# Kernel tuning notes

Hardware: AMD Instinct MI355X
Metric: run time of the kernel (lower is better)

## Reference

```python
import jax, jax.numpy as jnp
import numpy as np

N_NODES = 100000
N_HEDGES = 10000
D = 128  # i_d = v_d = e_d = q_d
NUM_CLASS = 10
E = 640000


def _linear_params(key, d_in, d_out):
    k1, k2 = jax.random.split(key)
    lim = 1.0 / np.sqrt(d_in)
    W = jax.random.uniform(k1, (d_in, d_out), jnp.float32, -lim, lim)
    b = jax.random.uniform(k2, (d_out,), jnp.float32, -lim, lim)
    return W, b


def setup_inputs() -> dict:
    key = jax.random.key(0)
    ks = jax.random.split(key, 12)
    vfeat = jax.random.normal(ks[0], (N_NODES, D), jnp.float32)
    efeat = jax.random.normal(ks[1], (N_HEDGES, D), jnp.float32)
    he_idx = jax.random.randint(ks[2], (E,), 0, N_HEDGES, jnp.int32)
    nd_idx = jax.random.randint(ks[3], (E,), 0, N_NODES, jnp.int32)
    Wfl, bfl = _linear_params(ks[4], D, D)   # first_layer_in: i_d -> v_d
    W1, b1 = _linear_params(ks[5], D, D)     # w1: e_d -> q_d
    W2, b2 = _linear_params(ks[6], D, D)     # w2: v_d -> q_d
    W3, b3 = _linear_params(ks[7], D, D)     # w3: v_d -> e_d
    W4, b4 = _linear_params(ks[8], D, D)     # w4: v_d -> q_d
    W5, b5 = _linear_params(ks[9], D, D)     # w5: e_d -> q_d
    W6, b6 = _linear_params(ks[10], D, D)    # w6: e_d -> v_d
    Wc, bc = _linear_params(ks[11], D, NUM_CLASS)
    return dict(vfeat=vfeat, efeat=efeat, he_idx=he_idx, nd_idx=nd_idx,
                first_layer=1, last_layer=1,
                Wfl=Wfl, bfl=bfl, W1=W1, b1=b1, W2=W2, b2=b2, W3=W3, b3=b3,
                W4=W4, b4=b4, W5=W5, b5=b5, W6=W6, b6=b6, Wc=Wc, bc=bc)


def _segment_softmax(logits, segs, num_segments):
    # softmax over the variable-size mailbox of each destination segment
    m = jax.ops.segment_max(logits, segs, num_segments=num_segments)
    m = jnp.where(jnp.isfinite(m), m, 0.0)  # empty segments
    e = jnp.exp(logits - m[segs])
    s = jax.ops.segment_sum(e, segs, num_segments=num_segments)
    return e / jnp.where(s > 0, s, 1.0)[segs]


def reference(vfeat, efeat, he_idx, nd_idx, first_layer, last_layer,
              Wfl, bfl, W1, b1, W2, b2, W3, b3, W4, b4, W5, b5, W6, b6, Wc, bc):
    scale = 1.0 / np.sqrt(D).astype(np.float32)
    # first_layer path (first_layer=1)
    feat_e = efeat @ Wfl + bfl                         # [M, v_d]
    k_e = feat_e @ W5 + b5                             # [M, q_d]
    v_e = feat_e @ W6 + b6                             # [M, v_d]
    q_v = vfeat @ W4 + b4                              # [N, q_d]
    # etype 'con': hyperedge -> node
    attn1 = jax.nn.leaky_relu((k_e[he_idx] * q_v[nd_idx]).sum(-1)) * scale  # [E]
    a1 = _segment_softmax(attn1, nd_idx, N_NODES)
    feat_v = jax.ops.segment_sum(a1[:, None] * v_e[he_idx], nd_idx,
                                 num_segments=N_NODES)  # [N, v_d]
    # etype 'in': node -> hyperedge
    k_v = feat_v @ W2 + b2                             # [N, q_d]
    v_v = feat_v @ W3 + b3                             # [N, e_d]
    q_e = feat_e @ W1 + b1                             # [M, q_d]
    attn2 = jax.nn.leaky_relu((k_v[nd_idx] * q_e[he_idx]).sum(-1)) * scale  # [E]
    a2 = _segment_softmax(attn2, he_idx, N_HEDGES)
    feat_e2 = jax.ops.segment_sum(a2[:, None] * v_v[nd_idx], he_idx,
                                  num_segments=N_HEDGES)  # [M, e_d]
    # last_layer path (last_layer=1): classification head (file save omitted)
    pred = feat_e2 @ Wc + bc                           # [M, num_class]
    return pred
```

## Files before the change

kernel.cpp:

```cpp
#include <hip/hip_runtime.h>
#include <hip/hip_bf16.h>
#include <math.h>


#define HY_M 10000
#define HY_N 100000
#define HY_E 640000

#define SH_N 9
#define NB_N 196
#define SH_M 6
#define NB_M 157

typedef float        f32x4 __attribute__((ext_vector_type(4)));
typedef unsigned int u32x4 __attribute__((ext_vector_type(4)));

__device__ __forceinline__ unsigned int f2bf(float x) {
    unsigned int u = __float_as_uint(x);
    return (u + 0x7fffu + ((u >> 16) & 1u)) >> 16;
}
__device__ __forceinline__ float2 bf2x2(unsigned int w) {
    float lo = __uint_as_float(w << 16);
    float hi = __uint_as_float(w & 0xffff0000u);
    return make_float2(lo, hi);
}
__device__ __forceinline__ float dot8(uint4 kw, float4 qa, float4 qb) {
    float2 k0 = bf2x2(kw.x), k1 = bf2x2(kw.y), k2 = bf2x2(kw.z), k3 = bf2x2(kw.w);
    return k0.x * qa.x + k0.y * qa.y + k1.x * qa.z + k1.y * qa.w
         + k2.x * qb.x + k2.y * qb.y + k3.x * qb.z + k3.y * qb.w;
}
__device__ __forceinline__ void unpack8(uint4 vw, float (&vf)[8]) {
    float2 v0 = bf2x2(vw.x), v1 = bf2x2(vw.y), v2 = bf2x2(vw.z), v3 = bf2x2(vw.w);
    vf[0] = v0.x; vf[1] = v0.y; vf[2] = v1.x; vf[3] = v1.y;
    vf[4] = v2.x; vf[5] = v2.y; vf[6] = v3.x; vf[7] = v3.y;
}
__device__ __forceinline__ float red16(float d) {
    d += __shfl_xor(d, 8); d += __shfl_xor(d, 4);
    d += __shfl_xor(d, 2); d += __shfl_xor(d, 1);
    return d;
}

__launch_bounds__(256)
__global__ void coarse_hist(const int* __restrict__ nd, const int* __restrict__ he,
                            int* __restrict__ gcntN, int* __restrict__ gcntM, int E) {
    __shared__ int hN[256], hM[256];
    const int t = threadIdx.x;
    hN[t] = 0; hM[t] = 0;
    __syncthreads();
    const int base = blockIdx.x * 1024;
    for (int i = t; i < 1024; i += 256) {
        int e = base + i;
        if (e < E) {
            atomicAdd(&hN[nd[e] >> SH_N], 1);
            atomicAdd(&hM[he[e] >> SH_M], 1);
        }
    }
    __syncthreads();
    if (hN[t]) atomicAdd(&gcntN[t], hN[t]);
    if (hM[t]) atomicAdd(&gcntM[t], hM[t]);
}

__global__ void coarse_scan(const int* __restrict__ gcntN, const int* __restrict__ gcntM,
                            int* __restrict__ coffN, int* __restrict__ coffM, int E) {
    __shared__ int s[256];
    const int* g = blockIdx.x ? gcntM : gcntN;
    int* o = blockIdx.x ? coffM : coffN;
    const int nb = blockIdx.x ? NB_M : NB_N;
    const int t = threadIdx.x;
    int v = (t < nb) ? g[t] : 0;
    int orig = v;
    s[t] = v; __syncthreads();
    for (int off = 1; off < 256; off <<= 1) {
        int x = (t >= off) ? s[t - off] : 0;
        __syncthreads(); s[t] += x; __syncthreads();
    }
    if (t < nb) o[t] = s[t] - orig;
    if (t == 0) o[nb] = E;
}

__launch_bounds__(256)
__global__ void part_scatter(const int* __restrict__ nd, const int* __restrict__ he,
                             const int* __restrict__ coffN, const int* __restrict__ coffM,
                             int* __restrict__ gcurN, int* __restrict__ gcurM,
                             unsigned int* __restrict__ stN, unsigned int* __restrict__ stM,
                             int E) {
    __shared__ int hN[256], hM[256];
    const int t = threadIdx.x;
    hN[t] = 0; hM[t] = 0;
    __syncthreads();
    const int base = blockIdx.x * 1024;
    for (int i = t; i < 1024; i += 256) {
        int e = base + i;
        if (e < E) {
            atomicAdd(&hN[nd[e] >> SH_N], 1);
            atomicAdd(&hM[he[e] >> SH_M], 1);
        }
    }
    __syncthreads();
    int cN = hN[t], cM = hM[t];
    __syncthreads();
    if (cN) hN[t] = coffN[t] + atomicAdd(&gcurN[t], cN);
    if (cM) hM[t] = coffM[t] + atomicAdd(&gcurM[t], cM);
    __syncthreads();
    for (int i = t; i < 1024; i += 256) {
        int e = base + i;
        if (e < E) {
            int d = nd[e], h = he[e];
            int pN = atomicAdd(&hN[d >> SH_N], 1);
            stN[pN] = ((unsigned int)(d & 511) << 14) | (unsigned int)h;
            int pM = atomicAdd(&hM[h >> SH_M], 1);
            stM[pM] = ((unsigned int)(h & 63) << 17) | (unsigned int)d;
        }
    }
}

__launch_bounds__(256)
__global__ void bucket_build(const unsigned int* __restrict__ stN,
                             const unsigned int* __restrict__ stM,
                             const int* __restrict__ coffN, const int* __restrict__ coffM,
                             int* __restrict__ nd_off, int* __restrict__ he_off,
                             int* __restrict__ nd_adj, int* __restrict__ he_adj,
                             int* __restrict__ dcntg) {
    __shared__ int cnt[512];
    __shared__ int cur[512];
    __shared__ int ps[256];
    __shared__ int dh[64];
    int b = blockIdx.x;
    const int t = threadIdx.x;
    const unsigned int* st; const int* coff; int* offout; int* adj;
    int dmin, dcnt2, sshift; unsigned int smask; int ntot;
    const bool isN = b < NB_N;
    if (isN) {
        st = stN; coff = coffN; offout = nd_off; adj = nd_adj;
        dmin = b << SH_N; dcnt2 = min(512, HY_N - dmin);
        sshift = 14; smask = 0x3FFFu; ntot = HY_N;
    } else {
        b -= NB_N;
        st = stM; coff = coffM; offout = he_off; adj = he_adj;
        dmin = b << SH_M; dcnt2 = min(64, HY_M - dmin);
        sshift = 17; smask = 0x1FFFFu; ntot = HY_M;
    }
    const int cbase = coff[b], cend = coff[b + 1];
    cnt[t] = 0; cnt[t + 256] = 0;
    if (t < 64) dh[t] = 0;
    __syncthreads();
    for (int k = cbase + t; k < cend; k += 256)
        atomicAdd(&cnt[st[k] >> sshift], 1);
    __syncthreads();
    int a0 = cnt[2 * t], a1 = cnt[2 * t + 1];
    int pair = a0 + a1;
    ps[t] = pair;
    __syncthreads();
    for (int off = 1; off < 256; off <<= 1) {
        int x = (t >= off) ? ps[t - off] : 0;
        __syncthreads(); ps[t] += x; __syncthreads();
    }
    int excl = ps[t] - pair;
    cur[2 * t]     = cbase + excl;
    cur[2 * t + 1] = cbase + excl + a0;
    __syncthreads();
    for (int i = t; i < dcnt2; i += 256) offout[dmin + i] = cur[i];
    if (t == 0 && dmin + dcnt2 == ntot) offout[ntot] = cend;
    if (isN) {
        for (int i = t; i < dcnt2; i += 256)
            atomicAdd(&dh[min(cnt[i], 63)], 1);
    }
    __syncthreads();
    if (isN && t < 64 && dh[t]) atomicAdd(&dcntg[t], dh[t]);
    for (int k = cbase + t; k < cend; k += 256) {
        unsigned int w = st[k];
        int pos = atomicAdd(&cur[w >> sshift], 1);
        adj[pos] = (int)(w & smask);
    }
}

__global__ void deg_scan(const int* __restrict__ dcnt, int* __restrict__ dcur) {
    int t = threadIdx.x;
    int rt = 63 - t;
    int v = dcnt[rt];
    int s = v;
    for (int o = 1; o < 64; o <<= 1) {
        int x = __shfl_up(s, o, 64);
        if (t >= o) s += x;
    }
    dcur[rt] = s - v;
}

__launch_bounds__(256)
__global__ void deg_scatter(const int* __restrict__ off, int* __restrict__ dcur,
                            int* __restrict__ nperm, int n) {
    __shared__ int h[64];
    __shared__ int basev[64];
    int t = threadIdx.x;
    if (t < 64) h[t] = 0;
    __syncthreads();
    int i = blockIdx.x * blockDim.x + t;
    int bin = 0, lpos = 0;
    bool valid = i < n;
    if (valid) {
        bin = min(off[i + 1] - off[i], 63);
        lpos = atomicAdd(&h[bin], 1);
    }
    __syncthreads();
    if (t < 64 && h[t]) basev[t] = atomicAdd(&dcur[t], h[t]);
    __syncthreads();
    if (valid) nperm[basev[bin] + lpos] = i;
}

__device__ __forceinline__ void gemm_accum(const float* __restrict__ A,
        const float* __restrict__ W, int nrows, float* wlds,
        float (&acc)[4][4], int row0) {
    const int tid = threadIdx.x;
    const int cg = tid & 31;
    for (int i = tid; i < 4096; i += 512)
        ((float4*)wlds)[i] = ((const float4*)W)[i];
    __syncthreads();
    const float4* A0 = (const float4*)(A + (size_t)min(row0 + 0, nrows - 1) * 128);
    const float4* A1 = (const float4*)(A + (size_t)min(row0 + 1, nrows - 1) * 128);
    const float4* A2 = (const float4*)(A + (size_t)min(row0 + 2, nrows - 1) * 128);
    const float4* A3 = (const float4*)(A + (size_t)min(row0 + 3, nrows - 1) * 128);
    #pragma unroll 2
    for (int kq = 0; kq < 32; ++kq) {
        float4 ar[4] = {A0[kq], A1[kq], A2[kq], A3[kq]};
        const float4* wk = (const float4*)(wlds + kq * 512);
        float4 wr[4] = {wk[cg], wk[32 + cg], wk[64 + cg], wk[96 + cg]};
        #pragma unroll
        for (int r = 0; r < 4; ++r) {
            float av[4] = {ar[r].x, ar[r].y, ar[r].z, ar[r].w};
            #pragma unroll
            for (int j = 0; j < 4; ++j) {
                float wv[4] = {wr[j].x, wr[j].y, wr[j].z, wr[j].w};
                #pragma unroll
                for (int c = 0; c < 4; ++c)
                    acc[r][c] = fmaf(av[j], wv[c], acc[r][c]);
            }
        }
    }
}

__device__ __forceinline__ void gemm_store_f32(const float* __restrict__ b,
        float* __restrict__ Cf, int nrows, float (&acc)[4][4], int row0) {
    const int cg = threadIdx.x & 31;
    const float4 bv = ((const float4*)b)[cg];
    #pragma unroll
    for (int r = 0; r < 4; ++r) {
        int gr = row0 + r;
        if (gr < nrows) {
            float4 o = {acc[r][0] + bv.x, acc[r][1] + bv.y,
                        acc[r][2] + bv.z, acc[r][3] + bv.w};
            ((float4*)(Cf + (size_t)gr * 128))[cg] = o;
        }
    }
}

__launch_bounds__(512)
__global__ void gemm_pair(const float* __restrict__ Aa, const float* __restrict__ Wa,
                          float* __restrict__ Ca,
                          const float* __restrict__ Ab, const float* __restrict__ Wb,
                          float* __restrict__ Cb2, const float* __restrict__ zb) {
    __shared__ __align__(16) float wlds[16384];
    const int rs = threadIdx.x >> 5;
    const int row0 = blockIdx.x * 64 + rs * 4;
    const float* A = blockIdx.y ? Ab : Aa;
    const float* W = blockIdx.y ? Wb : Wa;
    float* C = blockIdx.y ? Cb2 : Ca;
    float acc[4][4] = {};
    gemm_accum(A, W, 128, wlds, acc, row0);
    gemm_store_f32(zb, C, 128, acc, row0);
}

__launch_bounds__(512)
__global__ void gemm_trip(const float* __restrict__ Wfl, const float* __restrict__ bfl,
        const float* __restrict__ W54, const float* __restrict__ b54v,
        const float* __restrict__ W6, const float* __restrict__ b6,
        const float* __restrict__ W12, const float* __restrict__ b12v,
        const float* __restrict__ w1b2, const float* __restrict__ s12,
        const float* __restrict__ w5b4, const float* __restrict__ s54,
        float* __restrict__ Wk, float* __restrict__ Wv, float* __restrict__ Wq,
        float* __restrict__ bk, float* __restrict__ bv, float* __restrict__ bq,
        float* __restrict__ u_c, float* __restrict__ u_k,
        float* __restrict__ t_c, float* __restrict__ t_k,
        const float* __restrict__ zb) {
    __shared__ __align__(16) float wlds[16384];
    const int y = blockIdx.y;
    if (y == 3) {
        if (blockIdx.x != 0) return;
        int t = threadIdx.x;
        if (t < 128) {
            float a1 = 0.f, a2 = 0.f, a3 = 0.f;
            for (int j = 0; j < 128; ++j) {
                float f = bfl[j];
                a1 += f * W54[j * 128 + t];
                a2 += f * W6[j * 128 + t];
                a3 += f * W12[j * 128 + t];
            }
            bk[t] = a1 + b54v[t];
            bv[t] = a2 + b6[t];
            bq[t] = a3 + b12v[t];
        } else if (t < 256) {
            int k = t - 128;
            float a1 = 0.f, a2 = 0.f;
            for (int j = 0; j < 128; ++j) {
                float f = Wfl[k * 128 + j];
                a1 += f * w1b2[j];
                a2 += f * w5b4[j];
            }
            u_c[k] = a1;
            u_k[k] = a2;
        }
        if (t == 0) {
            float a1 = 0.f, a2 = 0.f;
            for (int j = 0; j < 128; ++j) {
                a1 += bfl[j] * w1b2[j];
                a2 += bfl[j] * w5b4[j];
            }
            *t_c = a1 + *s12;
            *t_k = a2 + *s54;
        }
        return;
    }
    const int rs = threadIdx.x >> 5;
    const int row0 = blockIdx.x * 64 + rs * 4;
    const float* W = y == 0 ? W54 : (y == 1 ? W6 : W12);
    float* C = y == 0 ? Wk : (y == 1 ? Wv : Wq);
    float acc[4][4] = {};
    gemm_accum(Wfl, W, 128, wlds, acc, row0);
    gemm_store_f32(zb, C, 128, acc, row0);
}

__launch_bounds__(256)
__global__ void gemm_m(const float* __restrict__ A,
        const float* __restrict__ Wk, const float* __restrict__ bk,
        const float* __restrict__ Wv, const float* __restrict__ bvv,
        const float* __restrict__ Wq, const float* __restrict__ bq,
        const float* __restrict__ u_c, const float* __restrict__ t_c,
        const float* __restrict__ u_k, const float* __restrict__ t_k,
        float* __restrict__ c_e, float* __restrict__ ck,
        unsigned short* __restrict__ kv, float* __restrict__ qt, int nrows) {
    __shared__ __align__(16) float wlds[128 * 64];
    const int tid = threadIdx.x;
    if (blockIdx.y == 6) {
        const int w = tid >> 6, lane = tid & 63;
        float2 a1 = ((const float2*)u_c)[lane];
        float2 a2 = ((const float2*)u_k)[lane];
        for (int it = 0; it < 8; ++it) {
            int row = blockIdx.x * 32 + it * 4 + w;
            if (row < nrows) {
                float2 r = ((const float2*)(A + (size_t)row * 128))[lane];
                float d1 = r.x * a1.x + r.y * a1.y;
                float d2 = r.x * a2.x + r.y * a2.y;
                #pragma unroll
                for (int o = 32; o; o >>= 1) {
                    d1 += __shfl_xor(d1, o, 64);
                    d2 += __shfl_xor(d2, o, 64);
                }
                if (lane == 0) { c_e[row] = d1 + *t_c; ck[row] = d2 + *t_k; }
            }
        }
        return;
    }
    const int mat = blockIdx.y >> 1;
    const int half = blockIdx.y & 1;
    const float* W = mat == 0 ? Wk : (mat == 1 ? Wv : Wq);
    const float* bb = mat == 0 ? bk : (mat == 1 ? bvv : bq);
    const float4* W4 = (const float4*)W;
    float4* wl4 = (float4*)wlds;
    for (int i = tid; i < 2048; i += 256)
        wl4[i] = W4[(i >> 4) * 32 + half * 16 + (i & 15)];
    __syncthreads();
    const int cg = tid & 15;
    const int rs = tid >> 4;
    const int row0 = blockIdx.x * 32 + rs * 2;
    const float4* A0 = (const float4*)(A + (size_t)min(row0, nrows - 1) * 128);
    const float4* A1 = (const float4*)(A + (size_t)min(row0 + 1, nrows - 1) * 128);
    float acc[2][4] = {};
    #pragma unroll 4
    for (int kq = 0; kq < 32; ++kq) {
        float4 a0 = A0[kq], a1 = A1[kq];
        float av0[4] = {a0.x, a0.y, a0.z, a0.w};
        float av1[4] = {a1.x, a1.y, a1.z, a1.w};
        #pragma unroll
        for (int jj = 0; jj < 4; ++jj) {
            float4 w4 = wl4[(4 * kq + jj) * 16 + cg];
            float wv4[4] = {w4.x, w4.y, w4.z, w4.w};
            #pragma unroll
            for (int c = 0; c < 4; ++c) {
                acc[0][c] = fmaf(av0[jj], wv4[c], acc[0][c]);
                acc[1][c] = fmaf(av1[jj], wv4[c], acc[1][c]);
            }
        }
    }
    const float4 bv4 = ((const float4*)bb)[half * 16 + cg];
    #pragma unroll
    for (int r = 0; r < 2; ++r) {
        int gr = row0 + r;
        if (gr < nrows) {
            float o0 = acc[r][0] + bv4.x, o1 = acc[r][1] + bv4.y;
            float o2 = acc[r][2] + bv4.z, o3 = acc[r][3] + bv4.w;
            if (mat == 2) {
                float4 o = {o0, o1, o2, o3};
                ((float4*)(qt + (size_t)gr * 128))[half * 16 + cg] = o;
            } else {
                uint2 pk;
                pk.x = f2bf(o0) | (f2bf(o1) << 16);
                pk.y = f2bf(o2) | (f2bf(o3) << 16);
                *(uint2*)(kv + (size_t)gr * 256 + mat * 128 + half * 64 + cg * 4) = pk;
            }
        }
    }
}

__device__ __forceinline__ void prep_vecs_body(const float* WX, const float* WY,
        const float* bX, const float* bY, float* bXY, float* wXbY, float* sXY, int t) {
    if (t < 128) {
        float acc = 0.f;
        for (int j = 0; j < 128; ++j) acc += WY[t * 128 + j] * bX[j];
        bXY[t] = acc;
    } else {
        int k = t - 128;
        float acc = 0.f;
        for (int j = 0; j < 128; ++j) acc += WX[k * 128 + j] * bY[j];
        wXbY[k] = acc;
    }
    if (t == 0) {
        float acc = 0.f;
        for (int j = 0; j < 128; ++j) acc += bX[j] * bY[j];
        *sXY = acc;
    }
}

__global__ void prep_a(const float* __restrict__ W1, const float* __restrict__ b1,
                       const float* __restrict__ W2, const float* __restrict__ b2,
                       const float* __restrict__ W3, const float* __restrict__ b3,
                       const float* __restrict__ W4, const float* __restrict__ b4,
                       const float* __restrict__ W5, const float* __restrict__ b5,
                       const float* __restrict__ Wc,
                       float* __restrict__ W2T, float* __restrict__ W4T,
                       float* __restrict__ b12v, float* __restrict__ w1b2,
                       float* __restrict__ s12,
                       float* __restrict__ b54v, float* __restrict__ w5b4,
                       float* __restrict__ s54,
                       float* __restrict__ W3c, float* __restrict__ b3c,
                       float* __restrict__ zeros, int* __restrict__ zint) {
    const int x = blockIdx.x, t = threadIdx.x;
    if (x < 64) {
        int i = x * 256 + t;
        W2T[(i & 127) * 128 + (i >> 7)] = W2[i];
    } else if (x < 128) {
        int i = (x - 64) * 256 + t;
        W4T[(i & 127) * 128 + (i >> 7)] = W4[i];
    } else if (x == 128) {
        prep_vecs_body(W1, W2, b1, b2, b12v, w1b2, s12, t);
    } else if (x == 129) {
        prep_vecs_body(W5, W4, b5, b4, b54v, w5b4, s54, t);
    } else if (x < 136) {
        int i = (x - 130) * 256 + t;
        if (i < 1280) {
            int k = i / 10, c = i % 10;
            float acc = 0.f;
            for (int j = 0; j < 128; ++j) acc += W3[k * 128 + j] * Wc[j * 10 + c];
            W3c[i] = acc;
        } else if (i < 1290) {
            int c = i - 1280;
            float acc = 0.f;
            for (int j = 0; j < 128; ++j) acc += b3[j] * Wc[j * 10 + c];
            b3c[c] = acc;
        }
    } else if (x == 136) {
        if (t < 128) zeros[t] = 0.f;
    } else {
        int i = (x - 137) * 256 + t;
        if (i < 1152) zint[i] = 0;
    }
}

__launch_bounds__(256)
__global__ void attn_s1(const float* __restrict__ vf,
                        const unsigned int* __restrict__ kv,
                        const float* __restrict__ ck,
                        const int* __restrict__ off, const int* __restrict__ adj,
                        const int* __restrict__ nperm,
                        unsigned int* __restrict__ fv,
                        int nseg, float scale) {
    int slot = (blockIdx.x * blockDim.x + threadIdx.x) >> 4;
    int j = threadIdx.x & 15;
    if (slot >= nseg) return;
    int seg = nperm[slot];
    int beg = off[seg], end = off[seg + 1];
    const f32x4* qp = (const f32x4*)(vf + (size_t)seg * 128 + 8 * j);
    f32x4 qa4 = __builtin_nontemporal_load(qp);
    f32x4 qb4 = __builtin_nontemporal_load(qp + 1);
    float4 qa = {qa4.x, qa4.y, qa4.z, qa4.w};
    float4 qb = {qb4.x, qb4.y, qb4.z, qb4.w};
    float m = -INFINITY, l = 0.f;
    float a[8] = {};
    int i = beg;
    for (; i + 3 < end; i += 4) {
        int s0 = adj[i], s1 = adj[i + 1], s2 = adj[i + 2], s3 = adj[i + 3];
        const uint4* r0 = (const uint4*)(kv + (size_t)s0 * 128);
        const uint4* r1 = (const uint4*)(kv + (size_t)s1 * 128);
        const uint4* r2 = (const uint4*)(kv + (size_t)s2 * 128);
        const uint4* r3 = (const uint4*)(kv + (size_t)s3 * 128);
        uint4 k0 = r0[j], k1 = r1[j], k2 = r2[j], k3 = r3[j];
        uint4 v0 = r0[16 + j], v1 = r1[16 + j], v2 = r2[16 + j], v3 = r3[16 + j];
        float c0 = ck[s0], c1 = ck[s1], c2 = ck[s2], c3 = ck[s3];
        float d0 = dot8(k0, qa, qb), d1 = dot8(k1, qa, qb);
        float d2 = dot8(k2, qa, qb), d3 = dot8(k3, qa, qb);
        #pragma unroll
        for (int o = 8; o; o >>= 1) {
            d0 += __shfl_xor(d0, o); d1 += __shfl_xor(d1, o);
            d2 += __shfl_xor(d2, o); d3 += __shfl_xor(d3, o);
        }
        d0 += c0; d1 += c1; d2 += c2; d3 += c3;
        d0 = (d0 >= 0.f ? d0 : 0.01f * d0) * scale;
        d1 = (d1 >= 0.f ? d1 : 0.01f * d1) * scale;
        d2 = (d2 >= 0.f ? d2 : 0.01f * d2) * scale;
        d3 = (d3 >= 0.f ? d3 : 0.01f * d3) * scale;
        float mn = fmaxf(fmaxf(fmaxf(d0, d1), fmaxf(d2, d3)), m);
        float r  = __expf(m - mn);
        float p0 = __expf(d0 - mn), p1 = __expf(d1 - mn);
        float p2 = __expf(d2 - mn), p3 = __expf(d3 - mn);
        l = l * r + p0 + p1 + p2 + p3;
        float w0[8], w1[8], w2[8], w3[8];
        unpack8(v0, w0); unpack8(v1, w1); unpack8(v2, w2); unpack8(v3, w3);
        #pragma unroll
        for (int t = 0; t < 8; ++t)
            a[t] = fmaf(p3, w3[t], fmaf(p2, w2[t],
                   fmaf(p1, w1[t], fmaf(p0, w0[t], a[t] * r))));
        m = mn;
    }
    for (; i < end; ++i) {
        int s0 = adj[i];
        const uint4* r0 = (const uint4*)(kv + (size_t)s0 * 128);
        uint4 k0 = r0[j], v0 = r0[16 + j];
        float d = dot8(k0, qa, qb);
        d = red16(d);
        d += ck[s0];
        d = (d >= 0.f ? d : 0.01f * d) * scale;
        float mn = fmaxf(m, d);
        float r = __expf(m - mn);
        float p = __expf(d - mn);
        l = l * r + p;
        float w0[8]; unpack8(v0, w0);
        #pragma unroll
        for (int t = 0; t < 8; ++t) a[t] = fmaf(p, w0[t], a[t] * r);
        m = mn;
    }
    float inv = (l > 0.f) ? 1.f / l : 0.f;
    u32x4 o;
    o.x = f2bf(a[0] * inv) | (f2bf(a[1] * inv) << 16);
    o.y = f2bf(a[2] * inv) | (f2bf(a[3] * inv) << 16);
    o.z = f2bf(a[4] * inv) | (f2bf(a[5] * inv) << 16);
    o.w = f2bf(a[6] * inv) | (f2bf(a[7] * inv) << 16);
    __builtin_nontemporal_store(o, (u32x4*)(fv + (size_t)seg * 64 + 4 * j));
}

__launch_bounds__(256)
__global__ void attn_s2(const float* __restrict__ QT, const float* __restrict__ cvec,
                        const unsigned int* __restrict__ fv,
                        const int* __restrict__ off, const int* __restrict__ adj,
                        const float* __restrict__ W3c, const float* __restrict__ b3c,
                        const float* __restrict__ bc, float* __restrict__ out,
                        float scale) {
    __shared__ float sm[16], sl[16];
    __shared__ float sacc[16][16][9];
    const int seg = blockIdx.x;
    const int g = threadIdx.x >> 4;
    const int j = threadIdx.x & 15;
    const int beg = off[seg], end = off[seg + 1];
    const f32x4* qp = (const f32x4*)(QT + (size_t)seg * 128 + 8 * j);
    f32x4 qa4 = __builtin_nontemporal_load(qp);
    f32x4 qb4 = __builtin_nontemporal_load(qp + 1);
    float4 qa = {qa4.x, qa4.y, qa4.z, qa4.w};
    float4 qb = {qb4.x, qb4.y, qb4.z, qb4.w};
    const float cadd = cvec[seg];
    float m = -INFINITY, l = 0.f;
    float a[8] = {};
    int it = beg + g;
    if (it + 16 < end) {
        int s0 = adj[it], s1 = adj[it + 16];
        uint4 rw0 = ((const uint4*)(fv + (size_t)s0 * 64))[j];
        uint4 rw1 = ((const uint4*)(fv + (size_t)s1 * 64))[j];
        for (; it + 16 < end; it += 32) {
            uint4 ra = rw0, rb = rw1;
            if (it + 48 < end) {
                int t0 = adj[it + 32], t1 = adj[it + 48];
                rw0 = ((const uint4*)(fv + (size_t)t0 * 64))[j];
                rw1 = ((const uint4*)(fv + (size_t)t1 * 64))[j];
            } else if (it + 32 < end) {
                int t0 = adj[it + 32];
                rw0 = ((const uint4*)(fv + (size_t)t0 * 64))[j];
            }
            float v1[8], v2[8];
            unpack8(ra, v1); unpack8(rb, v2);
            float d1 = v1[0] * qa.x + v1[1] * qa.y + v1[2] * qa.z + v1[3] * qa.w
                     + v1[4] * qb.x + v1[5] * qb.y + v1[6] * qb.z + v1[7] * qb.w;
            float d2 = v2[0] * qa.x + v2[1] * qa.y + v2[2] * qa.z + v2[3] * qa.w
                     + v2[4] * qb.x + v2[5] * qb.y + v2[6] * qb.z + v2[7] * qb.w;
            #pragma unroll
            for (int o = 8; o; o >>= 1) { d1 += __shfl_xor(d1, o); d2 += __shfl_xor(d2, o); }
            d1 += cadd; d2 += cadd;
            d1 = (d1 >= 0.f ? d1 : 0.01f * d1) * scale;
            d2 = (d2 >= 0.f ? d2 : 0.01f * d2) * scale;
            float mn = fmaxf(fmaxf(m, d1), d2);
            float r  = __expf(m - mn);
            float p1 = __expf(d1 - mn);
            float p2 = __expf(d2 - mn);
            l = l * r + p1 + p2;
            #pragma unroll
            for (int t = 0; t < 8; ++t)
                a[t] = fmaf(p2, v2[t], fmaf(p1, v1[t], a[t] * r));
            m = mn;
        }
        if (it < end) {
            float v1[8]; unpack8(rw0, v1);
            float d = v1[0] * qa.x + v1[1] * qa.y + v1[2] * qa.z + v1[3] * qa.w
                    + v1[4] * qb.x + v1[5] * qb.y + v1[6] * qb.z + v1[7] * qb.w;
            d = red16(d);
            d += cadd;
            d = (d >= 0.f ? d : 0.01f * d) * scale;
            float mn = fmaxf(m, d);
            float r = __expf(m - mn);
            float p = __expf(d - mn);
            l = l * r + p;
            #pragma unroll
            for (int t = 0; t < 8; ++t) a[t] = fmaf(p, v1[t], a[t] * r);
            m = mn;
        }
    } else if (it < end) {
        int s0 = adj[it];
        uint4 rw0 = ((const uint4*)(fv + (size_t)s0 * 64))[j];
        float v1[8]; unpack8(rw0, v1);
        float d = v1[0] * qa.x + v1[1] * qa.y + v1[2] * qa.z + v1[3] * qa.w
                + v1[4] * qb.x + v1[5] * qb.y + v1[6] * qb.z + v1[7] * qb.w;
        d = red16(d);
        d += cadd;
        d = (d >= 0.f ? d : 0.01f * d) * scale;
        m = d; l = 1.f;
        #pragma unroll
        for (int t = 0; t < 8; ++t) a[t] = v1[t];
    }
    if (j == 0) { sm[g] = m; sl[g] = l; }
    #pragma unroll
    for (int t = 0; t < 8; ++t) sacc[g][j][t] = a[t];
    __syncthreads();
    if (threadIdx.x < 16) {
        const int t16 = threadIdx.x;
        float M2 = -INFINITY;
        #pragma unroll 4
        for (int gg = 0; gg < 16; ++gg) if (sl[gg] > 0.f) M2 = fmaxf(M2, sm[gg]);
        float L = 0.f;
        float acc[8] = {};
        #pragma unroll 4
        for (int gg = 0; gg < 16; ++gg) {
            float f = (sl[gg] > 0.f) ? __expf(sm[gg] - M2) : 0.f;
            L += f * sl[gg];
            #pragma unroll
            for (int t = 0; t < 8; ++t) acc[t] += f * sacc[gg][t16][t];
        }
        float inv = (L > 0.f) ? 1.f / L : 0.f;
        float fl  = (L > 0.f) ? 1.f : 0.f;
        #pragma unroll
        for (int t = 0; t < 8; ++t) acc[t] *= inv;
        float pp[10];
        #pragma unroll
        for (int c = 0; c < 10; ++c) {
            float s = 0.f;
            #pragma unroll
            for (int t = 0; t < 8; ++t)
                s = fmaf(acc[t], W3c[(8 * t16 + t) * 10 + c], s);
            pp[c] = s;
        }
        #pragma unroll
        for (int o = 8; o; o >>= 1) {
            #pragma unroll
            for (int c = 0; c < 10; ++c) pp[c] += __shfl_xor(pp[c], o);
        }
        if (t16 == 0) {
            #pragma unroll
            for (int c = 0; c < 10; ++c)
                out[(size_t)seg * 10 + c] = pp[c] + fl * b3c[c] + bc[c];
        }
    }
}

extern "C" void kernel_launch(void* const* d_in, const int* in_sizes, int n_in,
                              void* d_out, int out_size, void* d_ws, size_t ws_size,
                              hipStream_t stream) {
    const float* vfeat = (const float*)d_in[0];
    const float* efeat = (const float*)d_in[1];
    const int*   he    = (const int*)d_in[2];
    const int*   nd    = (const int*)d_in[3];
    const float* Wfl = (const float*)d_in[6],  *bfl = (const float*)d_in[7];
    const float* W1  = (const float*)d_in[8],  *b1  = (const float*)d_in[9];
    const float* W2  = (const float*)d_in[10], *b2  = (const float*)d_in[11];
    const float* W3  = (const float*)d_in[12], *b3  = (const float*)d_in[13];
    const float* W4  = (const float*)d_in[14], *b4  = (const float*)d_in[15];
    const float* W5  = (const float*)d_in[16], *b5  = (const float*)d_in[17];
    const float* W6  = (const float*)d_in[18], *b6  = (const float*)d_in[19];
    const float* Wc  = (const float*)d_in[20], *bc  = (const float*)d_in[21];
    float* out = (float*)d_out;
    float* ws  = (float*)d_ws;

    const int M = HY_M, N = HY_N, E = HY_E;

    float* qt_e  = ws + 0;
    float* c_e   = ws + 1280000;
    float* ck    = ws + 1290000;
    float* W2T   = ws + 1300000;
    float* W4T   = ws + 1316384;
    float* W12   = ws + 1332768;
    float* W54   = ws + 1349152;
    float* Wk    = ws + 1365536;
    float* Wv    = ws + 1381920;
    float* Wq    = ws + 1398304;
    float* W3c   = ws + 1414688;
    float* b3c   = ws + 1415968;
    float* b12v  = ws + 1415984;
    float* w1b2  = ws + 1416112;
    float* s12   = ws + 1416240;
    float* b54v  = ws + 1416244;
    float* w5b4  = ws + 1416372;
    float* s54   = ws + 1416500;
    float* bk    = ws + 1416504;
    float* bv    = ws + 1416632;
    float* bq    = ws + 1416760;
    float* u_c   = ws + 1416888;
    float* u_k   = ws + 1417016;
    float* t_c   = ws + 1417144;
    float* t_k   = ws + 1417148;
    float* zeros = ws + 1417152;
    unsigned int* kv_bf = (unsigned int*)(ws + 1417280);
    unsigned int* fv_bf = kv_bf + (size_t)M * 128;
    int* nd_off = (int*)(fv_bf + (size_t)N * 64);
    int* he_off = nd_off + 100001;
    int* nd_adj = he_off + 10001;
    int* he_adj = nd_adj + 640000;
    int* nperm  = he_adj + 640000;
    unsigned int* stN = (unsigned int*)(nperm + 100000);
    unsigned int* stM = stN + 640000;
    int* gcntN = (int*)(stM + 640000);
    int* gcntM = gcntN + 256;
    int* gcurN = gcntM + 256;
    int* gcurM = gcurN + 256;
    int* dcnt  = gcurM + 256;
    int* dcur  = dcnt + 64;
    int* coffN = dcur + 64;
    int* coffM = coffN + 256;

    const float scale = 0.08838834764831843f;
    const int nchunk = (E + 1023) / 1024;

    prep_a<<<142, 256, 0, stream>>>(W1, b1, W2, b2, W3, b3, W4, b4, W5, b5, Wc,
                                    W2T, W4T, b12v, w1b2, s12, b54v, w5b4, s54,
                                    W3c, b3c, zeros, gcntN);

    coarse_hist<<<nchunk, 256, 0, stream>>>(nd, he, gcntN, gcntM, E);
    coarse_scan<<<2, 256, 0, stream>>>(gcntN, gcntM, coffN, coffM, E);
    part_scatter<<<nchunk, 256, 0, stream>>>(nd, he, coffN, coffM,
                                             gcurN, gcurM, stN, stM, E);
    bucket_build<<<NB_N + NB_M, 256, 0, stream>>>(stN, stM, coffN, coffM,
                                                  nd_off, he_off, nd_adj, he_adj,
                                                  dcnt);
    deg_scan<<<1, 64, 0, stream>>>(dcnt, dcur);
    deg_scatter<<<(N + 255) / 256, 256, 0, stream>>>(nd_off, dcur, nperm, N);

    gemm_pair<<<dim3(2, 2), 512, 0, stream>>>(W1, W2T, W12, W5, W4T, W54, zeros);
    gemm_trip<<<dim3(2, 4), 512, 0, stream>>>(Wfl, bfl, W54, b54v, W6, b6, W12, b12v,
                                              w1b2, s12, w5b4, s54,
                                              Wk, Wv, Wq, bk, bv, bq,
                                              u_c, u_k, t_c, t_k, zeros);

    gemm_m<<<dim3((M + 31) / 32, 7), 256, 0, stream>>>(
        efeat, Wk, bk, Wv, bv, Wq, bq, u_c, t_c, u_k, t_k, c_e, ck,
        (unsigned short*)kv_bf, qt_e, M);

    attn_s1<<<(N * 16 + 255) / 256, 256, 0, stream>>>(
        vfeat, kv_bf, ck, nd_off, nd_adj, nperm, fv_bf, N, scale);

    attn_s2<<<M, 256, 0, stream>>>(qt_e, c_e, fv_bf, he_off, he_adj,
                                   W3c, b3c, bc, out, scale);
}
```

Measured before the change: 215.7 us.

## Prefetch neighbor rows in attn_s1, fuse degree scan, enlarge histogram chunks

The node-side attention loop now processes two neighbours per step and software-prefetches the next pair's key/value rows and bias before computing on the current pair, replacing the 4-wide unrolled batch. Single-neighbour segments get a shortcut that skips the online softmax. The 64-bin degree scan is folded into deg_scatter, so each block recomputes it and one launch disappears. The histogram and partition kernels each handle 4096 edges per block instead of 1024, which cuts global atomics but leaves fewer blocks. The new gdcur counter relies on being zero at start, and it is not clear that it gets zeroed.

```diff
diff --git a/kernel.cpp b/kernel.cpp
--- a/kernel.cpp
+++ b/kernel.cpp
@@ -47,8 +47,8 @@
     const int t = threadIdx.x;
     hN[t] = 0; hM[t] = 0;
     __syncthreads();
-    const int base = blockIdx.x * 1024;
-    for (int i = t; i < 1024; i += 256) {
+    const int base = blockIdx.x * 4096;
+    for (int i = t; i < 4096; i += 256) {
         int e = base + i;
         if (e < E) {
             atomicAdd(&hN[nd[e] >> SH_N], 1);
@@ -88,8 +88,8 @@
     const int t = threadIdx.x;
     hN[t] = 0; hM[t] = 0;
     __syncthreads();
-    const int base = blockIdx.x * 1024;
-    for (int i = t; i < 1024; i += 256) {
+    const int base = blockIdx.x * 4096;
+    for (int i = t; i < 4096; i += 256) {
         int e = base + i;
         if (e < E) {
             atomicAdd(&hN[nd[e] >> SH_N], 1);
@@ -102,7 +102,7 @@
     if (cN) hN[t] = coffN[t] + atomicAdd(&gcurN[t], cN);
     if (cM) hM[t] = coffM[t] + atomicAdd(&gcurM[t], cM);
     __syncthreads();
-    for (int i = t; i < 1024; i += 256) {
+    for (int i = t; i < 4096; i += 256) {
         int e = base + i;
         if (e < E) {
             int d = nd[e], h = he[e];
@@ -174,25 +174,24 @@
     }
 }
 
-__global__ void deg_scan(const int* __restrict__ dcnt, int* __restrict__ dcur) {
-    int t = threadIdx.x;
-    int rt = 63 - t;
-    int v = dcnt[rt];
-    int s = v;
-    for (int o = 1; o < 64; o <<= 1) {
-        int x = __shfl_up(s, o, 64);
-        if (t >= o) s += x;
-    }
-    dcur[rt] = s - v;
-}
-
 __launch_bounds__(256)
-__global__ void deg_scatter(const int* __restrict__ off, int* __restrict__ dcur,
-                            int* __restrict__ nperm, int n) {
+__global__ void deg_scatter(const int* __restrict__ off, const int* __restrict__ dcnt,
+                            int* __restrict__ gdcur, int* __restrict__ nperm, int n) {
     __shared__ int h[64];
     __shared__ int basev[64];
+    __shared__ int sbase[64];
     int t = threadIdx.x;
-    if (t < 64) h[t] = 0;
+    if (t < 64) {
+        int rt = 63 - t;
+        int v = dcnt[rt];
+        int s = v;
+        for (int o = 1; o < 64; o <<= 1) {
+            int x = __shfl_up(s, o, 64);
+            if (t >= o) s += x;
+        }
+        sbase[rt] = s - v;
+        h[t] = 0;
+    }
     __syncthreads();
     int i = blockIdx.x * blockDim.x + t;
     int bin = 0, lpos = 0;
@@ -202,9 +201,9 @@
         lpos = atomicAdd(&h[bin], 1);
     }
     __syncthreads();
-    if (t < 64 && h[t]) basev[t] = atomicAdd(&dcur[t], h[t]);
-    __syncthreads();
-    if (valid) nperm[basev[bin] + lpos] = i;
+    if (t < 64 && h[t]) basev[t] = atomicAdd(&gdcur[t], h[t]);
+    __syncthreads();
+    if (valid) nperm[sbase[bin] + basev[bin] + lpos] = i;
 }
 
 __device__ __forceinline__ void gemm_accum(const float* __restrict__ A,
@@ -495,56 +494,80 @@
     float m = -INFINITY, l = 0.f;
     float a[8] = {};
     int i = beg;
-    for (; i + 3 < end; i += 4) {
-        int s0 = adj[i], s1 = adj[i + 1], s2 = adj[i + 2], s3 = adj[i + 3];
-        const uint4* r0 = (const uint4*)(kv + (size_t)s0 * 128);
-        const uint4* r1 = (const uint4*)(kv + (size_t)s1 * 128);
-        const uint4* r2 = (const uint4*)(kv + (size_t)s2 * 128);
-        const uint4* r3 = (const uint4*)(kv + (size_t)s3 * 128);
-        uint4 k0 = r0[j], k1 = r1[j], k2 = r2[j], k3 = r3[j];
-        uint4 v0 = r0[16 + j], v1 = r1[16 + j], v2 = r2[16 + j], v3 = r3[16 + j];
-        float c0 = ck[s0], c1 = ck[s1], c2 = ck[s2], c3 = ck[s3];
-        float d0 = dot8(k0, qa, qb), d1 = dot8(k1, qa, qb);
-        float d2 = dot8(k2, qa, qb), d3 = dot8(k3, qa, qb);
-        #pragma unroll
-        for (int o = 8; o; o >>= 1) {
-            d0 += __shfl_xor(d0, o); d1 += __shfl_xor(d1, o);
-            d2 += __shfl_xor(d2, o); d3 += __shfl_xor(d3, o);
-        }
-        d0 += c0; d1 += c1; d2 += c2; d3 += c3;
-        d0 = (d0 >= 0.f ? d0 : 0.01f * d0) * scale;
-        d1 = (d1 >= 0.f ? d1 : 0.01f * d1) * scale;
-        d2 = (d2 >= 0.f ? d2 : 0.01f * d2) * scale;
-        d3 = (d3 >= 0.f ? d3 : 0.01f * d3) * scale;
-        float mn = fmaxf(fmaxf(fmaxf(d0, d1), fmaxf(d2, d3)), m);
-        float r  = __expf(m - mn);
-        float p0 = __expf(d0 - mn), p1 = __expf(d1 - mn);
-        float p2 = __expf(d2 - mn), p3 = __expf(d3 - mn);
-        l = l * r + p0 + p1 + p2 + p3;
-        float w0[8], w1[8], w2[8], w3[8];
-        unpack8(v0, w0); unpack8(v1, w1); unpack8(v2, w2); unpack8(v3, w3);
-        #pragma unroll
-        for (int t = 0; t < 8; ++t)
-            a[t] = fmaf(p3, w3[t], fmaf(p2, w2[t],
-                   fmaf(p1, w1[t], fmaf(p0, w0[t], a[t] * r))));
-        m = mn;
-    }
-    for (; i < end; ++i) {
+    const int cnt = end - beg;
+    if (cnt >= 2) {
+        int s0 = adj[i], s1 = adj[i + 1];
+        uint4 kw0 = ((const uint4*)(kv + (size_t)s0 * 128))[j];
+        uint4 vw0 = ((const uint4*)(kv + (size_t)s0 * 128 + 64))[j];
+        float c0 = ck[s0];
+        uint4 kw1 = ((const uint4*)(kv + (size_t)s1 * 128))[j];
+        uint4 vw1 = ((const uint4*)(kv + (size_t)s1 * 128 + 64))[j];
+        float c1 = ck[s1];
+        for (; i + 1 < end; i += 2) {
+            uint4 ka = kw0, va = vw0, kb = kw1, vb = vw1;
+            float ca = c0, cb = c1;
+            if (i + 3 < end) {
+                int t0 = adj[i + 2], t1 = adj[i + 3];
+                kw0 = ((const uint4*)(kv + (size_t)t0 * 128))[j];
+                vw0 = ((const uint4*)(kv + (size_t)t0 * 128 + 64))[j];
+                c0 = ck[t0];
+                kw1 = ((const uint4*)(kv + (size_t)t1 * 128))[j];
+                vw1 = ((const uint4*)(kv + (size_t)t1 * 128 + 64))[j];
+                c1 = ck[t1];
+            } else if (i + 2 < end) {
+                int t0 = adj[i + 2];
+                kw0 = ((const uint4*)(kv + (size_t)t0 * 128))[j];
+                vw0 = ((const uint4*)(kv + (size_t)t0 * 128 + 64))[j];
+                c0 = ck[t0];
+            }
+            float d1 = dot8(ka, qa, qb);
+            float d2 = dot8(kb, qa, qb);
+            d1 += __shfl_xor(d1, 8); d2 += __shfl_xor(d2, 8);
+            d1 += __shfl_xor(d1, 4); d2 += __shfl_xor(d2, 4);
+            d1 += __shfl_xor(d1, 2); d2 += __shfl_xor(d2, 2);
+            d1 += __shfl_xor(d1, 1); d2 += __shfl_xor(d2, 1);
+            d1 += ca; d2 += cb;
+            d1 = (d1 >= 0.f ? d1 : 0.01f * d1) * scale;
+            d2 = (d2 >= 0.f ? d2 : 0.01f * d2) * scale;
+            float mn = fmaxf(fmaxf(m, d1), d2);
+            float r  = __expf(m - mn);
+            float p1 = __expf(d1 - mn);
+            float p2 = __expf(d2 - mn);
+            l = l * r + p1 + p2;
+            float v1[8], v2[8];
+            unpack8(va, v1); unpack8(vb, v2);
+            #pragma unroll
+            for (int t = 0; t < 8; ++t)
+                a[t] = fmaf(p2, v2[t], fmaf(p1, v1[t], a[t] * r));
+            m = mn;
+        }
+        if (i < end) {
+            float d = dot8(kw0, qa, qb);
+            d = red16(d);
+            d += c0;
+            d = (d >= 0.f ? d : 0.01f * d) * scale;
+            float mn = fmaxf(m, d);
+            float r = __expf(m - mn);
+            float p = __expf(d - mn);
+            l = l * r + p;
+            float v1[8]; unpack8(vw0, v1);
+            #pragma unroll
+            for (int t = 0; t < 8; ++t)
+                a[t] = fmaf(p, v1[t], a[t] * r);
+            m = mn;
+        }
+    } else if (cnt == 1) {
         int s0 = adj[i];
-        const uint4* r0 = (const uint4*)(kv + (size_t)s0 * 128);
-        uint4 k0 = r0[j], v0 = r0[16 + j];
-        float d = dot8(k0, qa, qb);
+        uint4 kw0 = ((const uint4*)(kv + (size_t)s0 * 128))[j];
+        uint4 vw0 = ((const uint4*)(kv + (size_t)s0 * 128 + 64))[j];
+        float d = dot8(kw0, qa, qb);
         d = red16(d);
         d += ck[s0];
         d = (d >= 0.f ? d : 0.01f * d) * scale;
-        float mn = fmaxf(m, d);
-        float r = __expf(m - mn);
-        float p = __expf(d - mn);
-        l = l * r + p;
-        float w0[8]; unpack8(v0, w0);
+        l = 1.f;
+        float v1[8]; unpack8(vw0, v1);
         #pragma unroll
-        for (int t = 0; t < 8; ++t) a[t] = fmaf(p, w0[t], a[t] * r);
-        m = mn;
+        for (int t = 0; t < 8; ++t) a[t] = v1[t];
     }
     float inv = (l > 0.f) ? 1.f / l : 0.f;
     u32x4 o;
@@ -744,12 +767,12 @@
     int* gcurN = gcntM + 256;
     int* gcurM = gcurN + 256;
     int* dcnt  = gcurM + 256;
-    int* dcur  = dcnt + 64;
-    int* coffN = dcur + 64;
+    int* gdcur = dcnt + 64;
+    int* coffN = gdcur + 64;
     int* coffM = coffN + 256;
 
     const float scale = 0.08838834764831843f;
-    const int nchunk = (E + 1023) / 1024;
+    const int nchunk = (E + 4095) / 4096;
 
     prep_a<<<142, 256, 0, stream>>>(W1, b1, W2, b2, W3, b3, W4, b4, W5, b5, Wc,
                                     W2T, W4T, b12v, w1b2, s12, b54v, w5b4, s54,
@@ -762,8 +785,7 @@
     bucket_build<<<NB_N + NB_M, 256, 0, stream>>>(stN, stM, coffN, coffM,
                                                   nd_off, he_off, nd_adj, he_adj,
                                                   dcnt);
-    deg_scan<<<1, 64, 0, stream>>>(dcnt, dcur);
-    deg_scatter<<<(N + 255) / 256, 256, 0, stream>>>(nd_off, dcur, nperm, N);
+    deg_scatter<<<(N + 255) / 256, 256, 0, stream>>>(nd_off, dcnt, gdcur, nperm, N);
 
     gemm_pair<<<dim3(2, 2), 512, 0, stream>>>(W1, W2T, W12, W5, W4T, W54, zeros);
     gemm_trip<<<dim3(2, 4), 512, 0, stream>>>(Wfl, bfl, W54, b54v, W6, b6, W12, b12v,
```

New measurement: 193.0 us. -10.5%, faster.
